# Kernel tuning notes

Measured on AMD Instinct MI355X. Metric: run time of the kernel, lower is better.

## Reference

```python
import jax, jax.numpy as jnp
import numpy as np
from jax import lax

N, C1, C2, H, W = 4, 256, 256, 80, 80
CH = 128           # c_ = int(c2 * e)
G, KS = 1, 3       # groups, kernel_size
K = KS * KS        # sampling points per group
PAD, DIL = 1, 1
EPS_BN, EPS_LN = 1e-5, 1e-6


def conv_bn_silu(x, w, g, b, m, v, stride=1):
    # ultralytics Conv: conv(bias=False) + BatchNorm2d(eval) + SiLU
    pad = (w.shape[2] - 1) // 2
    y = lax.conv_general_dilated(x, w, (stride, stride), [(pad, pad), (pad, pad)],
                                 dimension_numbers=('NCHW', 'OIHW', 'NCHW'))
    s = g / jnp.sqrt(v + EPS_BN)
    y = y * s[None, :, None, None] + (b - m * s)[None, :, None, None]
    return jax.nn.silu(y)


def dcnv3_core(x, offset, mask):
    # x: (N,H,W,C) NHWC; offset: (N,H,W,G*K*2); mask: (N,H,W,G,K) softmaxed over K
    n, h, w, c = x.shape
    gc = c // G
    xp = jnp.pad(x, ((0, 0), (PAD, PAD), (PAD, PAD), (0, 0)))
    Hp, Wp = h + 2 * PAD, w + 2 * PAD
    base = (DIL * (KS - 1)) // 2
    # reference points (normalized by padded spatial size), stride 1
    ref_x = (jnp.arange(w, dtype=x.dtype) + base + 0.5) / Wp   # (W,)
    ref_y = (jnp.arange(h, dtype=x.dtype) + base + 0.5) / Hp   # (H,)
    gx = (jnp.arange(KS, dtype=x.dtype) * DIL - base) / Wp
    gy = (jnp.arange(KS, dtype=x.dtype) * DIL - base) / Hp
    grid_x = jnp.repeat(gx, KS)   # point p = i*KS + j -> x = gx[i]
    grid_y = jnp.tile(gy, KS)     # y = gy[j]  (torch meshgrid 'ij' ordering)
    off = offset.reshape(n, h, w, G, K, 2)
    loc_x = ref_x[None, None, :, None, None] + grid_x + off[..., 0] / Wp
    loc_y = ref_y[None, :, None, None, None] + grid_y + off[..., 1] / Hp
    # grid_sample align_corners=False: pixel = norm * size - 0.5
    px = loc_x * Wp - 0.5
    py = loc_y * Hp - 0.5
    x0 = jnp.floor(px); y0 = jnp.floor(py)
    lw, lh = px - x0, py - y0
    x0i, y0i = x0.astype(jnp.int32), y0.astype(jnp.int32)
    xv = jnp.transpose(xp.reshape(n, Hp * Wp, G, gc), (0, 2, 1, 3))  # (N,G,S,gc)
    tw = lambda a: jnp.transpose(a, (0, 3, 1, 2, 4))[..., None]      # (N,H,W,G,K)->(N,G,H,W,K,1)

    def gather(yi, xi):
        valid = ((xi >= 0) & (xi < Wp) & (yi >= 0) & (yi < Hp)).astype(x.dtype)
        idx = jnp.clip(yi, 0, Hp - 1) * Wp + jnp.clip(xi, 0, Wp - 1)
        idx = jnp.transpose(idx, (0, 3, 1, 2, 4)).reshape(n, G, h * w * K)
        v = jnp.take_along_axis(xv, idx[..., None], axis=2).reshape(n, G, h, w, K, gc)
        return v * tw(valid)   # zeros padding_mode

    out = (gather(y0i, x0i) * tw((1 - lh) * (1 - lw))
           + gather(y0i, x0i + 1) * tw((1 - lh) * lw)
           + gather(y0i + 1, x0i) * tw(lh * (1 - lw))
           + gather(y0i + 1, x0i + 1) * tw(lh * lw))   # (N,G,H,W,K,gc)
    m = jnp.transpose(mask, (0, 3, 1, 2, 4))[..., None]
    out = (out * m).sum(axis=4)                        # (N,G,H,W,gc)
    return jnp.transpose(out, (0, 2, 3, 1, 4)).reshape(n, h, w, c)


def forward(x, w1, g1, b1, m1, v1, w2, g2, b2, m2, v2,
            dw_w, dw_b, ln_g, ln_b, off_w, off_b, msk_w, msk_b,
            in_w, in_b, out_w, out_b, g3, b3, m3, v3):
    y = conv_bn_silu(x, w1, g1, b1, m1, v1)   # cv1: 3x3 Conv c1->c_
    y = conv_bn_silu(y, w2, g2, b2, m2, v2)   # cv2.conv: 1x1 Conv c_->c2
    t = jnp.transpose(y, (0, 2, 3, 1))        # NHWC
    x_proj = t @ in_w.T + in_b                # input_proj
    # dw_conv: depthwise 3x3 -> LayerNorm (channels_last) -> GELU
    dw = lax.conv_general_dilated(y, dw_w, (1, 1), [(1, 1), (1, 1)],
                                  dimension_numbers=('NCHW', 'OIHW', 'NCHW'),
                                  feature_group_count=C2)
    dw = jnp.transpose(dw, (0, 2, 3, 1)) + dw_b
    mu = dw.mean(-1, keepdims=True)
    var = ((dw - mu) ** 2).mean(-1, keepdims=True)
    dw = (dw - mu) / jnp.sqrt(var + EPS_LN) * ln_g + ln_b
    dw = jax.nn.gelu(dw, approximate=False)
    offset = dw @ off_w.T + off_b                                       # (N,H,W,G*K*2)
    mask = jax.nn.softmax((dw @ msk_w.T + msk_b).reshape(N, H, W, G, K), axis=-1)
    z = dcnv3_core(x_proj, offset, mask)
    z = z @ out_w.T + out_b                   # output_proj
    z = jnp.transpose(z, (0, 3, 1, 2))        # NCHW
    s = g3 / jnp.sqrt(v3 + EPS_BN)
    z = z * s[None, :, None, None] + (b3 - m3 * s)[None, :, None, None]
    z = jax.nn.silu(z)
    return x + z                              # shortcut (c1 == c2)


def setup_inputs():
    key = jax.random.key(0)
    ks = jax.random.split(key, 16)
    r = lambda k, s, sc=0.05: jax.random.normal(k, s, dtype=jnp.float32) * sc
    return {
        'x': jax.random.normal(ks[0], (N, C1, H, W), dtype=jnp.float32),
        'w1': r(ks[1], (CH, C1, 3, 3)),
        'g1': jnp.ones((CH,), jnp.float32), 'b1': jnp.zeros((CH,), jnp.float32),
        'm1': r(ks[2], (CH,), 0.1),
        'v1': jax.random.uniform(ks[3], (CH,), jnp.float32, 0.5, 1.5),
        'w2': r(ks[4], (C2, CH, 1, 1)),
        'g2': jnp.ones((C2,), jnp.float32), 'b2': jnp.zeros((C2,), jnp.float32),
        'm2': r(ks[5], (C2,), 0.1),
        'v2': jax.random.uniform(ks[6], (C2,), jnp.float32, 0.5, 1.5),
        'dw_w': r(ks[7], (C2, 1, 3, 3)), 'dw_b': jnp.zeros((C2,), jnp.float32),
        'ln_g': jnp.ones((C2,), jnp.float32), 'ln_b': jnp.zeros((C2,), jnp.float32),
        'off_w': r(ks[8], (G * K * 2, C2), 0.01), 'off_b': jnp.zeros((G * K * 2,), jnp.float32),
        'msk_w': r(ks[9], (G * K, C2), 0.01), 'msk_b': jnp.zeros((G * K,), jnp.float32),
        'in_w': r(ks[10], (C2, C2)), 'in_b': jnp.zeros((C2,), jnp.float32),
        'out_w': r(ks[11], (C2, C2)), 'out_b': jnp.zeros((C2,), jnp.float32),
        'g3': jnp.ones((C2,), jnp.float32), 'b3': jnp.zeros((C2,), jnp.float32),
        'm3': r(ks[12], (C2,), 0.1),
        'v3': jax.random.uniform(ks[13], (C2,), jnp.float32, 0.5, 1.5),
    }


def reference(x, w1, g1, b1, m1, v1, w2, g2, b2, m2, v2,
              dw_w, dw_b, ln_g, ln_b, off_w, off_b, msk_w, msk_b,
              in_w, in_b, out_w, out_b, g3, b3, m3, v3):
    return forward(x, w1, g1, b1, m1, v1, w2, g2, b2, m2, v2,
                   dw_w, dw_b, ln_g, ln_b, off_w, off_b, msk_w, msk_b,
                   in_w, in_b, out_w, out_b, g3, b3, m3, v3)
```

## Files before the change

kernel.cpp:

```cpp
#include <hip/hip_runtime.h>
#include <cmath>

#define TN 4
#define TC1 256
#define TCH 128
#define TC2 256
#define TH 80
#define TW 80
#define THP 82
#define TWP 84
#define NPIX (TN*TH*TW)

#define OFF_WBF   0
#define OFF_W2B   294912
#define OFF_INWB  327680
#define OFF_OUTWB 393216
#define OFF_DWT   458752
#define OFF_WCAT  461056
#define OFF_WCATB 467968
#define OFF_T1    468128
#define OFF_T2    468512
#define OFF_T3P   469024
#define OFF_XPAD  469504
#define OFF_Y2N   7525888
#define OFF_RAWN  10802688
#define OFF_ZN    11493888

typedef __attribute__((ext_vector_type(8))) short bf16x8;
typedef __attribute__((ext_vector_type(4))) float f32x4;

__device__ __forceinline__ float siluf(float v) { return v / (1.f + expf(-v)); }
__device__ __forceinline__ short rnbf(float f) {
  unsigned u = __float_as_uint(f);
  unsigned r = (u + 0x7fffu + ((u >> 16) & 1u)) >> 16;
  return (short)r;
}
__device__ __forceinline__ float bf2f(short s) {
  return __uint_as_float(((unsigned)(unsigned short)s) << 16);
}

__global__ __launch_bounds__(256) void k_prep(
    const float* __restrict__ w1, const float* __restrict__ g1, const float* __restrict__ b1,
    const float* __restrict__ m1, const float* __restrict__ v1,
    const float* __restrict__ w2, const float* __restrict__ g2, const float* __restrict__ b2,
    const float* __restrict__ m2, const float* __restrict__ v2,
    const float* __restrict__ dww, const float* __restrict__ offw, const float* __restrict__ offb,
    const float* __restrict__ mskw, const float* __restrict__ mskb,
    const float* __restrict__ inw, const float* __restrict__ outw, const float* __restrict__ outb,
    const float* __restrict__ g3, const float* __restrict__ b3,
    const float* __restrict__ m3, const float* __restrict__ v3,
    const float* __restrict__ x, float* __restrict__ ws)
{
  __shared__ short lds[80 * 40];
  if (blockIdx.x >= 1836) {
    short* xpn = (short*)(ws + OFF_XPAD);
    int b = blockIdx.x - 1836;
    int cc = b & 7; int hp = (b >> 3) % THP; int n = b / (THP * 8);
    int c0 = cc * 32;
    int t = threadIdx.x;
    int h = hp - 1;
    bool hv = (h >= 0 && h < TH);
    if (hv) {
      for (int f = t; f < 640; f += 256) {
        int ci = f / 20; int w4 = (f - ci * 20) * 4;
        float4 xv = *(const float4*)(x + ((n * TC1 + c0 + ci) * TH + h) * TW + w4);
        lds[(w4 + 0) * 40 + ci] = rnbf(xv.x);
        lds[(w4 + 1) * 40 + ci] = rnbf(xv.y);
        lds[(w4 + 2) * 40 + ci] = rnbf(xv.z);
        lds[(w4 + 3) * 40 + ci] = rnbf(xv.w);
      }
    }
    __syncthreads();
    short* op = xpn + ((n * THP + hp) * TWP) * TC2 + c0;
    for (int g = t; g < 672; g += 256) {
      int ci4 = (g & 7) * 4; int wp = g >> 3;
      short4 v = {0, 0, 0, 0};
      if (hv && wp >= 1 && wp <= TW) v = *(const short4*)(&lds[(wp - 1) * 40 + ci4]);
      *(short4*)(op + wp * TC2 + ci4) = v;
    }
    return;
  }
  int i = blockIdx.x * 256 + threadIdx.x;
  if (i < 294912) {
    int co = i / 2304; int r = i - co * 2304;
    int tap = r >> 8; int ci = r & 255; int ky = tap / 3; int kx = tap - ky * 3;
    float s = g1[co] * __frsqrt_rn(v1[co] + 1e-5f);
    ((short*)(ws + OFF_WBF))[i] = rnbf(w1[((co * TC1 + ci) * 3 + ky) * 3 + kx] * s);
    return;
  }
  i -= 294912;
  if (i < 32768) {
    int co = i >> 7; int ci = i & 127;
    float s = g2[co] * __frsqrt_rn(v2[co] + 1e-5f);
    ((short*)(ws + OFF_W2B))[i] = rnbf(w2[co * TCH + ci] * s);
    return;
  }
  i -= 32768;
  if (i < 65536) {
    int co = i >> 8; int ci = i & 255;
    ((short*)(ws + OFF_INWB))[i] = rnbf(inw[co * TC2 + ci]);
    return;
  }
  i -= 65536;
  if (i < 65536) {
    int co = i >> 8; int ci = i & 255;
    float s = g3[co] * __frsqrt_rn(v3[co] + 1e-5f);
    ((short*)(ws + OFF_OUTWB))[i] = rnbf(outw[co * TC2 + ci] * s);
    return;
  }
  i -= 65536;
  if (i < 2304) { int c = i & 255; int j = i >> 8; ws[OFF_DWT + i] = dww[c * 9 + j]; return; }
  i -= 2304;
  if (i < 8192) {
    int c = i & 255; int j = i >> 8;
    float v = 0.f;
    if (j < 18) v = offw[j * 256 + c];
    else if (j < 27) v = mskw[(j - 18) * 256 + c];
    ((short*)(ws + OFF_WCAT))[i] = rnbf(v);
    return;
  }
  i -= 8192;
  if (i < 27) { ws[OFF_WCATB + i] = (i < 18) ? offb[i] : mskb[i - 18]; return; }
  i -= 27;
  if (i < 128) { float s = g1[i] / sqrtf(v1[i] + 1e-5f); ws[OFF_T1 + i] = b1[i] - m1[i] * s; return; }
  i -= 128;
  if (i < 256) { float s = g2[i] / sqrtf(v2[i] + 1e-5f); ws[OFF_T2 + i] = b2[i] - m2[i] * s; return; }
  i -= 256;
  if (i < 256) { float s = g3[i] / sqrtf(v3[i] + 1e-5f); ws[OFF_T3P + i] = outb[i] * s + b3[i] - m3[i] * s; return; }
}

#define BH_STR 40
#define BH_PIX 108
#define BH_ELE (BH_PIX * BH_STR)
#define Y1_STR 136
__global__ __launch_bounds__(256) void k_cv12(const short* __restrict__ xpn, const short* __restrict__ wbf,
                                              const short* __restrict__ w2b,
                                              const float* __restrict__ t1v, const float* __restrict__ t2v,
                                              short* __restrict__ y2b)
{
  __shared__ short U[64 * Y1_STR];

  int b = blockIdx.x;
  int wt = b % 5; b /= 5; int ht = b % 20; int n = b / 20;
  int w0 = wt * 16, h0 = ht * 4;

  int tid = threadIdx.x;
  int wave = tid >> 6, lane = tid & 63;
  int ln = lane & 15, q = lane >> 4;
  int co0 = wave * 32;

  int u0 = tid, u1 = tid + 256;
  int p0 = u0 >> 2, s0 = u0 & 3;
  int p1 = u1 >> 2, s1 = u1 & 3;
  int hh0 = p0 / 18, ww0 = p0 - hh0 * 18;
  int hh1 = p1 / 18, ww1 = p1 - hh1 * 18;
  const short* sb0 = xpn + ((n * THP + h0 + hh0) * TWP + (w0 + ww0)) * 256 + s0 * 8;
  const short* sb1 = xpn + ((n * THP + h0 + hh1) * TWP + (w0 + ww1)) * 256 + s1 * 8;
  bool hasu1 = (u1 < 432);
  int d0 = p0 * BH_STR + s0 * 8;
  int d1 = p1 * BH_STR + s1 * 8;

  const short* abase = wbf + (co0 + ln) * 2304 + q * 8;

  f32x4 acc[2][4];
#pragma unroll
  for (int i = 0; i < 2; ++i)
#pragma unroll
    for (int j = 0; j < 4; ++j) acc[i][j] = (f32x4){0.f, 0.f, 0.f, 0.f};

  bf16x8 rb0 = *(const bf16x8*)(sb0);
  bf16x8 rb1 = {0, 0, 0, 0, 0, 0, 0, 0};
  if (hasu1) rb1 = *(const bf16x8*)(sb1);
  *(bf16x8*)(&U[d0]) = rb0;
  if (hasu1) *(bf16x8*)(&U[d1]) = rb1;
  __syncthreads();

  for (int cc = 0; cc < 8; ++cc) {
    int cur = cc & 1;
    bf16x8 af[9][2];
#pragma unroll
    for (int tap = 0; tap < 9; ++tap)
#pragma unroll
      for (int mt = 0; mt < 2; ++mt)
        af[tap][mt] = *(const bf16x8*)(abase + (mt * 16) * 2304 + tap * 256 + cc * 32);
    if (cc < 7) {
      rb0 = *(const bf16x8*)(sb0 + (cc + 1) * 32);
      if (hasu1) rb1 = *(const bf16x8*)(sb1 + (cc + 1) * 32);
    }
#pragma unroll
    for (int tap = 0; tap < 9; ++tap) {
      const int ky = tap / 3, kx = tap - (tap / 3) * 3;
      bf16x8 bv[4];
#pragma unroll
      for (int nt = 0; nt < 4; ++nt) {
        int pr = nt * 16 + ln;
        int hr = pr >> 4, wc = pr & 15;
        bv[nt] = *(const bf16x8*)(&U[cur * BH_ELE + ((hr + ky) * 18 + (wc + kx)) * BH_STR + q * 8]);
      }
#pragma unroll
      for (int mt = 0; mt < 2; ++mt)
#pragma unroll
        for (int nt = 0; nt < 4; ++nt)
          acc[mt][nt] = __builtin_amdgcn_mfma_f32_16x16x32_bf16(af[tap][mt], bv[nt], acc[mt][nt], 0, 0, 0);
    }
    if (cc < 7) {
      *(bf16x8*)(&U[(cur ^ 1) * BH_ELE + d0]) = rb0;
      if (hasu1) *(bf16x8*)(&U[(cur ^ 1) * BH_ELE + d1]) = rb1;
      __syncthreads();
    }
  }

  __syncthreads();
#pragma unroll
  for (int mt = 0; mt < 2; ++mt) {
    int co = co0 + mt * 16 + q * 4;
    float t0 = t1v[co], t1 = t1v[co + 1], t2 = t1v[co + 2], t3 = t1v[co + 3];
#pragma unroll
    for (int nt = 0; nt < 4; ++nt) {
      int px = nt * 16 + ln;
      short4 p;
      p.x = rnbf(siluf(acc[mt][nt][0] + t0));
      p.y = rnbf(siluf(acc[mt][nt][1] + t1));
      p.z = rnbf(siluf(acc[mt][nt][2] + t2));
      p.w = rnbf(siluf(acc[mt][nt][3] + t3));
      *(short4*)(&U[px * Y1_STR + co]) = p;
    }
  }
  __syncthreads();

  int coh2 = wave * 64;
  const short* a2base = w2b + (coh2 + ln) * TCH + q * 8;

  f32x4 acc2[4][4];
#pragma unroll
  for (int i = 0; i < 4; ++i)
#pragma unroll
    for (int j = 0; j < 4; ++j) acc2[i][j] = (f32x4){0.f, 0.f, 0.f, 0.f};

#pragma unroll
  for (int c = 0; c < 4; ++c) {
    bf16x8 a2[4], b2[4];
#pragma unroll
    for (int mt = 0; mt < 4; ++mt)
      a2[mt] = *(const bf16x8*)(a2base + (mt * 16) * TCH + c * 32);
#pragma unroll
    for (int nt = 0; nt < 4; ++nt)
      b2[nt] = *(const bf16x8*)(&U[(nt * 16 + ln) * Y1_STR + c * 32 + q * 8]);
#pragma unroll
    for (int mt = 0; mt < 4; ++mt)
#pragma unroll
      for (int nt = 0; nt < 4; ++nt)
        acc2[mt][nt] = __builtin_amdgcn_mfma_f32_16x16x32_bf16(a2[mt], b2[nt], acc2[mt][nt], 0, 0, 0);
  }

#pragma unroll
  for (int mt = 0; mt < 4; ++mt) {
    int co = coh2 + mt * 16 + q * 4;
    float t0 = t2v[co], t1 = t2v[co + 1], t2 = t2v[co + 2], t3 = t2v[co + 3];
#pragma unroll
    for (int nt = 0; nt < 4; ++nt) {
      int pr = nt * 16 + ln;
      int hr = pr >> 4, wc = pr & 15;
      int pix = (n * TH + h0 + hr) * TW + (w0 + wc);
      short4 p;
      p.x = rnbf(siluf(acc2[mt][nt][0] + t0));
      p.y = rnbf(siluf(acc2[mt][nt][1] + t1));
      p.z = rnbf(siluf(acc2[mt][nt][2] + t2));
      p.w = rnbf(siluf(acc2[mt][nt][3] + t3));
      *(short4*)(y2b + pix * TC2 + co) = p;
    }
  }
}

#define A_STR 40
#define DT_STR 264
__global__ __launch_bounds__(256) void k_pidw(
    const short* __restrict__ y2b, const short* __restrict__ inwb, const float* __restrict__ inb,
    short* __restrict__ xproj,
    const float* __restrict__ dwt, const float* __restrict__ dwb, const float* __restrict__ lng,
    const float* __restrict__ lnb, const short* __restrict__ wcatb16, const float* __restrict__ wcatb,
    float* __restrict__ raw)
{
  __shared__ short smem[4 * 128 * A_STR];

  int tid = threadIdx.x;
  int wave = tid >> 6, lane = tid & 63;

  if (blockIdx.x < 400) {
    short (*As)[128 * A_STR] = (short(*)[128 * A_STR])(smem);
    short (*Bs)[128 * A_STR] = (short(*)[128 * A_STR])(smem + 2 * 128 * A_STR);

    int b = blockIdx.x;
    int ch = b & 1; int pt = b >> 1;
    int co_base = ch * 128;
    int pix0 = pt * 128;

    int ln = lane & 15, q = lane >> 4;
    int coh = (wave & 1) * 64;
    int pxh = (wave >> 1) * 64;

    int srow = tid >> 1;
    int ssub = (tid & 1) * 16;
    const short* arow = inwb + (co_base + srow) * TC2 + ssub;
    const short* brow = y2b + (pix0 + srow) * TC2 + ssub;

    f32x4 acc[4][4];
#pragma unroll
    for (int i = 0; i < 4; ++i)
#pragma unroll
      for (int j = 0; j < 4; ++j) acc[i][j] = (f32x4){0.f, 0.f, 0.f, 0.f};

    bf16x8 ra0, ra1, rb0, rb1;
    auto grab = [&](int c) {
      const short* ap = arow + c * 32;
      const short* bp = brow + c * 32;
      ra0 = *(const bf16x8*)(ap);
      ra1 = *(const bf16x8*)(ap + 8);
      rb0 = *(const bf16x8*)(bp);
      rb1 = *(const bf16x8*)(bp + 8);
    };
    auto put = [&](int buf) {
      int o = srow * A_STR + ssub;
      *(bf16x8*)(&As[buf][o])     = ra0;
      *(bf16x8*)(&As[buf][o + 8]) = ra1;
      *(bf16x8*)(&Bs[buf][o])     = rb0;
      *(bf16x8*)(&Bs[buf][o + 8]) = rb1;
    };
    auto comp = [&](int buf) {
      bf16x8 af[4], bfv[4];
#pragma unroll
      for (int mt = 0; mt < 4; ++mt)
        af[mt] = *(const bf16x8*)(&As[buf][(coh + mt * 16 + ln) * A_STR + q * 8]);
#pragma unroll
      for (int nt = 0; nt < 4; ++nt)
        bfv[nt] = *(const bf16x8*)(&Bs[buf][(pxh + nt * 16 + ln) * A_STR + q * 8]);
#pragma unroll
      for (int mt = 0; mt < 4; ++mt)
#pragma unroll
        for (int nt = 0; nt < 4; ++nt)
          acc[mt][nt] = __builtin_amdgcn_mfma_f32_16x16x32_bf16(af[mt], bfv[nt], acc[mt][nt], 0, 0, 0);
    };

    const int NCH = TC2 / 32;
    grab(0);
    put(0);
    __syncthreads();
    for (int c = 0; c < NCH; ++c) {
      if (c < NCH - 1) grab(c + 1);
      comp(c & 1);
      if (c < NCH - 1) {
        __syncthreads();
        put((c + 1) & 1);
        __syncthreads();
      }
    }

#pragma unroll
    for (int mt = 0; mt < 4; ++mt) {
      int co = co_base + coh + mt * 16 + q * 4;
      float b0 = inb[co], b1 = inb[co + 1], b2 = inb[co + 2], b3 = inb[co + 3];
#pragma unroll
      for (int nt = 0; nt < 4; ++nt) {
        int pix = pix0 + pxh + nt * 16 + ln;
        short4 p;
        p.x = rnbf(acc[mt][nt][0] + b0);
        p.y = rnbf(acc[mt][nt][1] + b1);
        p.z = rnbf(acc[mt][nt][2] + b2);
        p.w = rnbf(acc[mt][nt][3] + b3);
        *(short4*)(xproj + pix * TC2 + co) = p;
      }
    }
    return;
  }

  short* dt = smem;

  int half = lane >> 5;
  int c0 = (lane & 31) * 8;
  int pix0 = (blockIdx.x - 400) * 32;

  float4 db0 = *(const float4*)(dwb + c0);
  float4 db1 = *(const float4*)(dwb + c0 + 4);
  float4 g0 = *(const float4*)(lng + c0);
  float4 g1 = *(const float4*)(lng + c0 + 4);
  float4 lb0 = *(const float4*)(lnb + c0);
  float4 lb1 = *(const float4*)(lnb + c0 + 4);
  float gv[8] = {g0.x, g0.y, g0.z, g0.w, g1.x, g1.y, g1.z, g1.w};
  float bvv[8] = {lb0.x, lb0.y, lb0.z, lb0.w, lb1.x, lb1.y, lb1.z, lb1.w};
  const float is2 = 0.70710678118654752f;

  for (int r = 0; r < 4; ++r) {
    int pl = wave * 8 + half * 4 + r;
    int pix = pix0 + pl;
    int w = pix % TW; int h = (pix / TW) % TH; int n = pix / (TH * TW);
    float v[8] = {db0.x, db0.y, db0.z, db0.w, db1.x, db1.y, db1.z, db1.w};
#pragma unroll
    for (int dy = 0; dy < 3; ++dy) {
#pragma unroll
      for (int dx = 0; dx < 3; ++dx) {
        int hh = h + dy - 1, ww = w + dx - 1;
        bool ok = (hh >= 0) & (hh < TH) & (ww >= 0) & (ww < TW);
        int off = ok ? (((n * TH + hh) * TW + ww) * TC2 + c0) : c0;
        bf16x8 yv = *(const bf16x8*)(y2b + off);
        float m = ok ? 1.f : 0.f;
        const float* wp = dwt + (dy * 3 + dx) * TC2 + c0;
        float4 w0 = *(const float4*)(wp);
        float4 w1 = *(const float4*)(wp + 4);
        v[0] += bf2f(yv[0]) * w0.x * m;
        v[1] += bf2f(yv[1]) * w0.y * m;
        v[2] += bf2f(yv[2]) * w0.z * m;
        v[3] += bf2f(yv[3]) * w0.w * m;
        v[4] += bf2f(yv[4]) * w1.x * m;
        v[5] += bf2f(yv[5]) * w1.y * m;
        v[6] += bf2f(yv[6]) * w1.z * m;
        v[7] += bf2f(yv[7]) * w1.w * m;
      }
    }
    float sv = 0.f, sq = 0.f;
#pragma unroll
    for (int i = 0; i < 8; ++i) { sv += v[i]; sq += v[i] * v[i]; }
#pragma unroll
    for (int o = 16; o > 0; o >>= 1) { sv += __shfl_xor(sv, o); sq += __shfl_xor(sq, o); }
    float mu = sv * (1.f / 256.f);
    float var = sq * (1.f / 256.f) - mu * mu;
    float rs = 1.f / sqrtf(var + 1e-6f);
    bf16x8 o8;
#pragma unroll
    for (int i = 0; i < 8; ++i) {
      float nv = (v[i] - mu) * rs * gv[i] + bvv[i];
      o8[i] = rnbf(0.5f * nv * (1.f + erff(nv * is2)));
    }
    *(bf16x8*)(&dt[pl * DT_STR + c0]) = o8;
  }
  __syncthreads();

  int ln = lane & 15, q = lane >> 4;
  int g = wave & 1;
  int jbase = (wave >> 1) * 16;

  f32x4 acc = {0.f, 0.f, 0.f, 0.f};
  const short* ap = wcatb16 + (jbase + ln) * 256 + q * 8;
  const short* bp = &dt[(g * 16 + ln) * DT_STR + q * 8];
#pragma unroll
  for (int kk = 0; kk < 256; kk += 32) {
    bf16x8 a  = *(const bf16x8*)(ap + kk);
    bf16x8 bf = *(const bf16x8*)(bp + kk);
    acc = __builtin_amdgcn_mfma_f32_16x16x32_bf16(a, bf, acc, 0, 0, 0);
  }

  int pix = pix0 + g * 16 + ln;
#pragma unroll
  for (int r = 0; r < 4; ++r) {
    int j = jbase + q * 4 + r;
    if (j < 27) raw[pix * 27 + j] = acc[r] + wcatb[j];
  }
}

__global__ __launch_bounds__(256) void k_dcn(const short* __restrict__ xproj, const float* __restrict__ raw,
                                             short* __restrict__ z)
{
  __shared__ int2 sp[8][36];
  int tid = threadIdx.x;
  int pixbase = blockIdx.x * 8;

  for (int j = tid; j < 288; j += 256) {
    int pxl = j / 36, t = j - pxl * 36;
    int pix = pixbase + pxl;
    int w = pix % TW; int h = (pix / TW) % TH;
    const float* r = raw + pix * 27;
    int k = t >> 2, tap = t & 3;
    int tx = tap & 1, ty = tap >> 1;
    float mx = r[18];
#pragma unroll
    for (int kk = 1; kk < 9; ++kk) mx = fmaxf(mx, r[18 + kk]);
    float sum = 0.f, ek = 0.f;
#pragma unroll
    for (int kk = 0; kk < 9; ++kk) {
      float ee = expf(r[18 + kk] - mx);
      sum += ee;
      if (kk == k) ek = ee;
    }
    float mk = ek / sum;
    float px = (float)(w + k / 3) + r[2 * k];
    float py = (float)(h + k % 3) + r[2 * k + 1];
    float x0f = floorf(px), y0f = floorf(py);
    float lw = px - x0f, lh = py - y0f;
    int x0 = (int)x0f + tx, y0 = (int)y0f + ty;
    float wt = mk * (tx ? lw : 1.f - lw) * (ty ? lh : 1.f - lh);
    bool valid = (x0 >= 1) & (x0 <= TW) & (y0 >= 1) & (y0 <= TH);
    int2 pr;
    pr.x = valid ? (((y0 - 1) * TW + (x0 - 1)) * TC2) : 0;
    pr.y = valid ? __float_as_int(wt) : 0;
    sp[pxl][t] = pr;
  }
  __syncthreads();

  int wave = tid >> 6, lane = tid & 63;
  int half = lane >> 5;
  int pxl = wave * 2 + half;
  int pix = pixbase + pxl;
  int n = pix / (TH * TW);
  int c0 = (lane & 31) * 8;
  const short* xb = xproj + n * (TH * TW * TC2) + c0;

  float a[8] = {0.f, 0.f, 0.f, 0.f, 0.f, 0.f, 0.f, 0.f};
#pragma unroll
  for (int t = 0; t < 36; ++t) {
    int2 pr = sp[pxl][t];
    float wt = __int_as_float(pr.y);
    bf16x8 v = *(const bf16x8*)(xb + pr.x);
#pragma unroll
    for (int i = 0; i < 8; ++i) a[i] += wt * bf2f(v[i]);
  }
  bf16x8 o8;
#pragma unroll
  for (int i = 0; i < 8; ++i) o8[i] = rnbf(a[i]);
  *(bf16x8*)(z + pix * TC2 + c0) = o8;
}

__global__ __launch_bounds__(256) void k_proj_out(const short* __restrict__ zb, const short* __restrict__ outwb,
                                                  const float* __restrict__ t3p,
                                                  const float* __restrict__ x, float* __restrict__ out)
{
  __shared__ short As[2][128 * A_STR];
  __shared__ short Bs[2][128 * A_STR];

  int b = blockIdx.x;
  int ch = b & 1; int pt = b >> 1;
  int co_base = ch * 128;
  int pix0 = pt * 128;

  int tid = threadIdx.x;
  int wave = tid >> 6, lane = tid & 63;
  int ln = lane & 15, q = lane >> 4;
  int coh = (wave & 1) * 64;
  int pxh = (wave >> 1) * 64;

  int srow = tid >> 1;
  int ssub = (tid & 1) * 16;
  const short* arow = outwb + (co_base + srow) * TC2 + ssub;
  const short* brow = zb + (pix0 + srow) * TC2 + ssub;

  f32x4 acc[4][4];
#pragma unroll
  for (int i = 0; i < 4; ++i)
#pragma unroll
    for (int j = 0; j < 4; ++j) acc[i][j] = (f32x4){0.f, 0.f, 0.f, 0.f};

  bf16x8 ra0, ra1, rb0, rb1;
  auto grab = [&](int c) {
    const short* ap = arow + c * 32;
    const short* bp = brow + c * 32;
    ra0 = *(const bf16x8*)(ap);
    ra1 = *(const bf16x8*)(ap + 8);
    rb0 = *(const bf16x8*)(bp);
    rb1 = *(const bf16x8*)(bp + 8);
  };
  auto put = [&](int buf) {
    int o = srow * A_STR + ssub;
    *(bf16x8*)(&As[buf][o])     = ra0;
    *(bf16x8*)(&As[buf][o + 8]) = ra1;
    *(bf16x8*)(&Bs[buf][o])     = rb0;
    *(bf16x8*)(&Bs[buf][o + 8]) = rb1;
  };
  auto comp = [&](int buf) {
    bf16x8 af[4], bfv[4];
#pragma unroll
    for (int mt = 0; mt < 4; ++mt)
      af[mt] = *(const bf16x8*)(&As[buf][(coh + mt * 16 + ln) * A_STR + q * 8]);
#pragma unroll
    for (int nt = 0; nt < 4; ++nt)
      bfv[nt] = *(const bf16x8*)(&Bs[buf][(pxh + nt * 16 + ln) * A_STR + q * 8]);
#pragma unroll
    for (int mt = 0; mt < 4; ++mt)
#pragma unroll
      for (int nt = 0; nt < 4; ++nt)
        acc[mt][nt] = __builtin_amdgcn_mfma_f32_16x16x32_bf16(af[mt], bfv[nt], acc[mt][nt], 0, 0, 0);
  };

  const int NCH = TC2 / 32;
  grab(0);
  put(0);
  __syncthreads();
  for (int c = 0; c < NCH; ++c) {
    if (c < NCH - 1) grab(c + 1);
    comp(c & 1);
    if (c < NCH - 1) {
      __syncthreads();
      put((c + 1) & 1);
      __syncthreads();
    }
  }

  __syncthreads();
  float* tb = (float*)(&As[0][0]);
  float* wb = tb + wave * 1056;
  int pixw = pix0 + pxh;
  int nn = pixw / (TH * TW);
  int hw0 = pixw - nn * (TH * TW);

#pragma unroll
  for (int mt = 0; mt < 4; ++mt) {
#pragma unroll
    for (int nt = 0; nt < 4; ++nt)
#pragma unroll
      for (int r = 0; r < 4; ++r)
        wb[(q * 4 + r) * 66 + nt * 16 + ln] = acc[mt][nt][r];
    int co = co_base + coh + mt * 16;
#pragma unroll
    for (int cl = 0; cl < 16; ++cl) {
      float vv = wb[cl * 66 + lane];
      int addr = (nn * TC2 + co + cl) * (TH * TW) + hw0 + lane;
      out[addr] = x[addr] + siluf(vv + t3p[co + cl]);
    }
  }
}

extern "C" void kernel_launch(void* const* d_in, const int* in_sizes, int n_in,
                              void* d_out, int out_size, void* d_ws, size_t ws_size,
                              hipStream_t stream)
{
  const float* x    = (const float*)d_in[0];
  const float* w1   = (const float*)d_in[1];
  const float* g1   = (const float*)d_in[2];
  const float* b1   = (const float*)d_in[3];
  const float* m1   = (const float*)d_in[4];
  const float* v1   = (const float*)d_in[5];
  const float* w2   = (const float*)d_in[6];
  const float* g2   = (const float*)d_in[7];
  const float* b2   = (const float*)d_in[8];
  const float* m2   = (const float*)d_in[9];
  const float* v2   = (const float*)d_in[10];
  const float* dww  = (const float*)d_in[11];
  const float* dwb  = (const float*)d_in[12];
  const float* lng  = (const float*)d_in[13];
  const float* lnb  = (const float*)d_in[14];
  const float* offw = (const float*)d_in[15];
  const float* offb = (const float*)d_in[16];
  const float* mskw = (const float*)d_in[17];
  const float* mskb = (const float*)d_in[18];
  const float* inw  = (const float*)d_in[19];
  const float* inb  = (const float*)d_in[20];
  const float* outw = (const float*)d_in[21];
  const float* outb = (const float*)d_in[22];
  const float* g3   = (const float*)d_in[23];
  const float* b3   = (const float*)d_in[24];
  const float* m3   = (const float*)d_in[25];
  const float* v3   = (const float*)d_in[26];

  float* ws  = (float*)d_ws;
  float* out = (float*)d_out;

  short* xpn    = (short*)(ws + OFF_XPAD);
  short* wbf    = (short*)(ws + OFF_WBF);
  short* w2b    = (short*)(ws + OFF_W2B);
  short* inwb   = (short*)(ws + OFF_INWB);
  short* outwb  = (short*)(ws + OFF_OUTWB);
  short* wcat16 = (short*)(ws + OFF_WCAT);
  short* y2b    = (short*)(ws + OFF_Y2N);
  float* raw    = ws + OFF_RAWN;
  short* zb     = (short*)(ws + OFF_ZN);
  short* xproj  = (short*)d_out;

  hipLaunchKernelGGL(k_prep, dim3(1836 + TN * THP * 8), dim3(256), 0, stream,
                     w1, g1, b1, m1, v1, w2, g2, b2, m2, v2,
                     dww, offw, offb, mskw, mskb, inw, outw, outb, g3, b3, m3, v3, x, ws);
  hipLaunchKernelGGL(k_cv12,     dim3(400),   dim3(256), 0, stream, xpn, wbf, w2b,
                     ws + OFF_T1, ws + OFF_T2, y2b);
  hipLaunchKernelGGL(k_pidw,     dim3(1200),  dim3(256), 0, stream, y2b, inwb, inb, xproj,
                     ws + OFF_DWT, dwb, lng, lnb, wcat16, ws + OFF_WCATB, raw);
  hipLaunchKernelGGL(k_dcn,      dim3(3200),  dim3(256), 0, stream, xproj, raw, zb);
  hipLaunchKernelGGL(k_proj_out, dim3(400),   dim3(256), 0, stream, zb, outwb, ws + OFF_T3P, x, out);
}
```

Before: 269.0 us.

## Fuse deformable sampling with output projection and residual epilogue

Merges the DCN sampling kernel and the output-projection GEMM kernel into one. Each block samples 16 pixels into a shared-memory bf16 tile, then runs MFMA against the output weights straight from global memory and writes the BN+SiLU+residual result. This drops the global round-trip of the intermediate z tensor and one kernel launch. It also moves xproj out of the output buffer into workspace. The costs are that the small 16-pixel tile reloads the full weight matrix per block, and the epilogue stores only 16 contiguous floats per channel row, which hurts coalescing.

```diff
diff --git a/kernel.cpp b/kernel.cpp
--- a/kernel.cpp
+++ b/kernel.cpp
@@ -24,7 +24,7 @@
 #define OFF_XPAD  469504
 #define OFF_Y2N   7525888
 #define OFF_RAWN  10802688
-#define OFF_ZN    11493888
+#define OFF_XPJ   11493888
 
 typedef __attribute__((ext_vector_type(8))) short bf16x8;
 typedef __attribute__((ext_vector_type(4))) float f32x4;
@@ -456,14 +456,18 @@
   }
 }
 
-__global__ __launch_bounds__(256) void k_dcn(const short* __restrict__ xproj, const float* __restrict__ raw,
-                                             short* __restrict__ z)
+__global__ __launch_bounds__(256) void k_dcnpo(const short* __restrict__ xproj, const float* __restrict__ raw,
+                                               const short* __restrict__ outwb, const float* __restrict__ t3p,
+                                               const float* __restrict__ x, float* __restrict__ out)
 {
-  __shared__ int2 sp[8][36];
+  __shared__ int2 sp[16][36];
+  __shared__ short zt[16 * DT_STR];
+
   int tid = threadIdx.x;
-  int pixbase = blockIdx.x * 8;
-
-  for (int j = tid; j < 288; j += 256) {
+  int pixbase = blockIdx.x * 16;
+  int n = pixbase / (TH * TW);
+
+  for (int j = tid; j < 576; j += 256) {
     int pxl = j / 36, t = j - pxl * 36;
     int pix = pixbase + pxl;
     int w = pix % TW; int h = (pix / TW) % TH;
@@ -497,121 +501,53 @@
 
   int wave = tid >> 6, lane = tid & 63;
   int half = lane >> 5;
-  int pxl = wave * 2 + half;
-  int pix = pixbase + pxl;
-  int n = pix / (TH * TW);
   int c0 = (lane & 31) * 8;
   const short* xb = xproj + n * (TH * TW * TC2) + c0;
 
-  float a[8] = {0.f, 0.f, 0.f, 0.f, 0.f, 0.f, 0.f, 0.f};
-#pragma unroll
-  for (int t = 0; t < 36; ++t) {
-    int2 pr = sp[pxl][t];
-    float wt = __int_as_float(pr.y);
-    bf16x8 v = *(const bf16x8*)(xb + pr.x);
-#pragma unroll
-    for (int i = 0; i < 8; ++i) a[i] += wt * bf2f(v[i]);
-  }
-  bf16x8 o8;
-#pragma unroll
-  for (int i = 0; i < 8; ++i) o8[i] = rnbf(a[i]);
-  *(bf16x8*)(z + pix * TC2 + c0) = o8;
-}
-
-__global__ __launch_bounds__(256) void k_proj_out(const short* __restrict__ zb, const short* __restrict__ outwb,
-                                                  const float* __restrict__ t3p,
-                                                  const float* __restrict__ x, float* __restrict__ out)
-{
-  __shared__ short As[2][128 * A_STR];
-  __shared__ short Bs[2][128 * A_STR];
-
-  int b = blockIdx.x;
-  int ch = b & 1; int pt = b >> 1;
-  int co_base = ch * 128;
-  int pix0 = pt * 128;
-
-  int tid = threadIdx.x;
-  int wave = tid >> 6, lane = tid & 63;
+  for (int r = 0; r < 2; ++r) {
+    int pxl = wave * 4 + half * 2 + r;
+    float a[8] = {0.f, 0.f, 0.f, 0.f, 0.f, 0.f, 0.f, 0.f};
+#pragma unroll
+    for (int t = 0; t < 36; ++t) {
+      int2 pr = sp[pxl][t];
+      float wt = __int_as_float(pr.y);
+      bf16x8 v = *(const bf16x8*)(xb + pr.x);
+#pragma unroll
+      for (int i = 0; i < 8; ++i) a[i] += wt * bf2f(v[i]);
+    }
+    bf16x8 o8;
+#pragma unroll
+    for (int i = 0; i < 8; ++i) o8[i] = rnbf(a[i]);
+    *(bf16x8*)(&zt[pxl * DT_STR + c0]) = o8;
+  }
+  __syncthreads();
+
   int ln = lane & 15, q = lane >> 4;
-  int coh = (wave & 1) * 64;
-  int pxh = (wave >> 1) * 64;
-
-  int srow = tid >> 1;
-  int ssub = (tid & 1) * 16;
-  const short* arow = outwb + (co_base + srow) * TC2 + ssub;
-  const short* brow = zb + (pix0 + srow) * TC2 + ssub;
-
-  f32x4 acc[4][4];
-#pragma unroll
-  for (int i = 0; i < 4; ++i)
-#pragma unroll
-    for (int j = 0; j < 4; ++j) acc[i][j] = (f32x4){0.f, 0.f, 0.f, 0.f};
-
-  bf16x8 ra0, ra1, rb0, rb1;
-  auto grab = [&](int c) {
-    const short* ap = arow + c * 32;
-    const short* bp = brow + c * 32;
-    ra0 = *(const bf16x8*)(ap);
-    ra1 = *(const bf16x8*)(ap + 8);
-    rb0 = *(const bf16x8*)(bp);
-    rb1 = *(const bf16x8*)(bp + 8);
-  };
-  auto put = [&](int buf) {
-    int o = srow * A_STR + ssub;
-    *(bf16x8*)(&As[buf][o])     = ra0;
-    *(bf16x8*)(&As[buf][o + 8]) = ra1;
-    *(bf16x8*)(&Bs[buf][o])     = rb0;
-    *(bf16x8*)(&Bs[buf][o + 8]) = rb1;
-  };
-  auto comp = [&](int buf) {
-    bf16x8 af[4], bfv[4];
-#pragma unroll
-    for (int mt = 0; mt < 4; ++mt)
-      af[mt] = *(const bf16x8*)(&As[buf][(coh + mt * 16 + ln) * A_STR + q * 8]);
-#pragma unroll
-    for (int nt = 0; nt < 4; ++nt)
-      bfv[nt] = *(const bf16x8*)(&Bs[buf][(pxh + nt * 16 + ln) * A_STR + q * 8]);
-#pragma unroll
-    for (int mt = 0; mt < 4; ++mt)
-#pragma unroll
-      for (int nt = 0; nt < 4; ++nt)
-        acc[mt][nt] = __builtin_amdgcn_mfma_f32_16x16x32_bf16(af[mt], bfv[nt], acc[mt][nt], 0, 0, 0);
-  };
-
-  const int NCH = TC2 / 32;
-  grab(0);
-  put(0);
-  __syncthreads();
-  for (int c = 0; c < NCH; ++c) {
-    if (c < NCH - 1) grab(c + 1);
-    comp(c & 1);
-    if (c < NCH - 1) {
-      __syncthreads();
-      put((c + 1) & 1);
-      __syncthreads();
-    }
-  }
-
-  __syncthreads();
-  float* tb = (float*)(&As[0][0]);
-  float* wb = tb + wave * 1056;
-  int pixw = pix0 + pxh;
-  int nn = pixw / (TH * TW);
-  int hw0 = pixw - nn * (TH * TW);
-
+  int co0 = wave * 64;
+  const short* a2base = outwb + (co0 + ln) * TC2 + q * 8;
+
+  f32x4 acc[4];
+#pragma unroll
+  for (int i = 0; i < 4; ++i) acc[i] = (f32x4){0.f, 0.f, 0.f, 0.f};
+
+#pragma unroll
+  for (int c = 0; c < 8; ++c) {
+    bf16x8 bv = *(const bf16x8*)(&zt[ln * DT_STR + c * 32 + q * 8]);
+#pragma unroll
+    for (int mt = 0; mt < 4; ++mt) {
+      bf16x8 av = *(const bf16x8*)(a2base + (mt * 16) * TC2 + c * 32);
+      acc[mt] = __builtin_amdgcn_mfma_f32_16x16x32_bf16(av, bv, acc[mt], 0, 0, 0);
+    }
+  }
+
+  int hw0 = pixbase - n * (TH * TW);
 #pragma unroll
   for (int mt = 0; mt < 4; ++mt) {
-#pragma unroll
-    for (int nt = 0; nt < 4; ++nt)
-#pragma unroll
-      for (int r = 0; r < 4; ++r)
-        wb[(q * 4 + r) * 66 + nt * 16 + ln] = acc[mt][nt][r];
-    int co = co_base + coh + mt * 16;
-#pragma unroll
-    for (int cl = 0; cl < 16; ++cl) {
-      float vv = wb[cl * 66 + lane];
-      int addr = (nn * TC2 + co + cl) * (TH * TW) + hw0 + lane;
-      out[addr] = x[addr] + siluf(vv + t3p[co + cl]);
+    int co = co0 + mt * 16 + q * 4;
+#pragma unroll
+    for (int r = 0; r < 4; ++r) {
+      int addr = (n * TC2 + co + r) * (TH * TW) + hw0 + ln;
+      out[addr] = x[addr] + siluf(acc[mt][r] + t3p[co + r]);
     }
   }
 }
@@ -659,8 +595,7 @@
   short* wcat16 = (short*)(ws + OFF_WCAT);
   short* y2b    = (short*)(ws + OFF_Y2N);
   float* raw    = ws + OFF_RAWN;
-  short* zb     = (short*)(ws + OFF_ZN);
-  short* xproj  = (short*)d_out;
+  short* xproj  = (short*)(ws + OFF_XPJ);
 
   hipLaunchKernelGGL(k_prep, dim3(1836 + TN * THP * 8), dim3(256), 0, stream,
                      w1, g1, b1, m1, v1, w2, g2, b2, m2, v2,
@@ -669,6 +604,6 @@
                      ws + OFF_T1, ws + OFF_T2, y2b);
   hipLaunchKernelGGL(k_pidw,     dim3(1200),  dim3(256), 0, stream, y2b, inwb, inb, xproj,
                      ws + OFF_DWT, dwb, lng, lnb, wcat16, ws + OFF_WCATB, raw);
-  hipLaunchKernelGGL(k_dcn,      dim3(3200),  dim3(256), 0, stream, xproj, raw, zb);
-  hipLaunchKernelGGL(k_proj_out, dim3(400),   dim3(256), 0, stream, zb, outwb, ws + OFF_T3P, x, out);
+  hipLaunchKernelGGL(k_dcnpo,    dim3(1600),  dim3(256), 0, stream, xproj, raw, outwb,
+                     ws + OFF_T3P, x, out);
 }
```

Measured after the change: 279.1 us. 1.04x slower.
